# Optimization experiments

Hardware: AMD Instinct MI355X
Metric: run time of the kernel (lower is better)

The kernel has to match this reference:

```python
import jax, jax.numpy as jnp
import numpy as np


def fps(pts, m):
    # pts: [N,3]; iterative farthest point sampling, deterministic start at index 0
    d0 = jnp.sum((pts - pts[0]) ** 2, axis=-1)  # [N]
    def step(mind, _):
        nxt = jnp.argmax(mind)
        d = jnp.sum((pts - pts[nxt]) ** 2, axis=-1)
        return jnp.minimum(mind, d), nxt
    _, idxs = jax.lax.scan(step, d0, None, length=m - 1)
    return jnp.concatenate([jnp.zeros((1,), idxs.dtype), idxs])  # [m]


def knn(queries, pts, k):
    # queries [M,3], pts [N,3] -> [M,k] indices of k nearest points (includes self)
    d = (jnp.sum(queries ** 2, -1, keepdims=True)
         - 2.0 * queries @ pts.T
         + jnp.sum(pts ** 2, -1)[None, :])  # [M,N]
    _, idx = jax.lax.top_k(-d, k)
    return idx


def mlp(x, params):
    # shared PointNet MLP: Linear+ReLU stack
    for w, b in params:
        x = jax.nn.relu(x @ w + b)
    return x


def sa_level(points, feats, ratio, k, params):
    # set-abstraction: fps downsample -> knn group -> shared MLP -> max pool per cluster
    B, N, _ = points.shape
    m = int(N * ratio)
    sel = jax.vmap(lambda p: fps(p, m))(points)                      # [B,m]
    npts = jnp.take_along_axis(points, sel[..., None], axis=1)       # [B,m,3]
    nbr = jax.vmap(knn, in_axes=(0, 0, None))(npts, points, k)       # [B,m,k]
    C = feats.shape[-1]
    kf = jnp.take_along_axis(feats, nbr.reshape(B, m * k, 1), axis=1).reshape(B, m, k, C)
    h = mlp(kf, params)                                              # [B,m,k,out]
    return npts, jnp.max(h, axis=2)                                  # [B,m,3], [B,m,out]


def setup_inputs() -> dict:
    key = jax.random.key(0)
    ks = jax.random.split(key, 20)
    points = jax.random.normal(ks[0], (8, 8192, 3), dtype=jnp.float32)
    batch = jnp.repeat(jnp.arange(8, dtype=jnp.int64), 8192)
    dims = {
        'pn1': [(3, 8), (8, 16), (16, 16)],
        'pn2': [(16, 32), (32, 64), (64, 64)],
        'pn3': [(64, 128), (128, 256), (256, 256)],
    }
    inp = {'points': points, 'batch': batch}
    i = 1
    for name, shapes in dims.items():
        for j, (cin, cout) in enumerate(shapes, start=1):
            inp[f'{name}_w{j}'] = jax.random.normal(ks[i], (cin, cout), dtype=jnp.float32) * (1.0 / np.sqrt(cin))
            inp[f'{name}_b{j}'] = jnp.zeros((cout,), dtype=jnp.float32)
            i += 1
    return inp


def reference(points, batch,
              pn1_w1, pn1_b1, pn1_w2, pn1_b2, pn1_w3, pn1_b3,
              pn2_w1, pn2_b1, pn2_w2, pn2_b2, pn2_w3, pn2_b3,
              pn3_w1, pn3_b1, pn3_w2, pn3_b2, pn3_w3, pn3_b3):
    # batch is implied by the uniform [B,N,3] layout (all clouds equal size)
    p1 = [(pn1_w1, pn1_b1), (pn1_w2, pn1_b2), (pn1_w3, pn1_b3)]
    p2 = [(pn2_w1, pn2_b1), (pn2_w2, pn2_b2), (pn2_w3, pn2_b3)]
    p3 = [(pn3_w1, pn3_b1), (pn3_w2, pn3_b2), (pn3_w3, pn3_b3)]
    pts1, f1 = sa_level(points, points, 0.25, 4, p1)   # [8,2048,3], [8,2048,16]
    pts2, f2 = sa_level(pts1, f1, 0.25, 4, p2)         # [8,512,3], [8,512,64]
    # level 3: cluster == batch -> global max pool per cloud
    out = jnp.max(mlp(f2, p3), axis=1)                  # [8,256]
    return out
```

## Files before the change

kernel.cpp:

```cpp
#include <hip/hip_runtime.h>
#include <stdint.h>

typedef unsigned long long u64;
typedef unsigned int u32;
typedef float f2 __attribute__((ext_vector_type(2)));

__device__ __forceinline__ float rn_mul(float a, float b){ return __fmul_rn(a,b); }
__device__ __forceinline__ float rn_add(float a, float b){ return __fadd_rn(a,b); }
__device__ __forceinline__ float rn_sub(float a, float b){ return __fsub_rn(a,b); }

__device__ __forceinline__ float sq3(float dx, float dy, float dz){
  return rn_add(rn_add(rn_mul(dx,dx), rn_mul(dy,dy)), rn_mul(dz,dz));
}

__device__ __forceinline__ u32 fkey(float d){
  u32 b = __float_as_uint(d);
  return b ^ ((u32)((int)b >> 31) | 0x80000000u);
}
__device__ __forceinline__ float unfkey(u32 k){
  const u32 b = (k & 0x80000000u) ? (k ^ 0x80000000u) : ~k;
  return __uint_as_float(b);
}

__device__ __forceinline__ u64 shfl_xor64(u64 v, int mask){
  int lo = __shfl_xor((int)(u32)v, mask, 64);
  int hi = __shfl_xor((int)(u32)(v >> 32), mask, 64);
  return ((u64)(u32)hi << 32) | (u32)lo;
}
__device__ __forceinline__ u64 umin64(u64 a, u64 b){ return a < b ? a : b; }
__device__ __forceinline__ u64 umax64(u64 a, u64 b){ return a > b ? a : b; }

template<int C>
__device__ __forceinline__ u32 dstep(u32 v){
  u32 x = (u32)__builtin_amdgcn_update_dpp((int)v, (int)v, C, 0xF, 0xF, false);
  return x > v ? x : v;
}
__device__ __forceinline__ u32 wave64_maxu(u32 v){
  v = dstep<0x111>(v);
  v = dstep<0x112>(v);
  v = dstep<0x114>(v);
  v = dstep<0x118>(v);
  v = dstep<0x142>(v);
  v = dstep<0x143>(v);
  return (u32)__builtin_amdgcn_readlane((int)v, 63);
}
template<int C>
__device__ __forceinline__ u64 dstep64(u64 v){
  const u32 l = (u32)__builtin_amdgcn_update_dpp((int)(u32)v, (int)(u32)v, C, 0xF, 0xF, false);
  const u32 h = (u32)__builtin_amdgcn_update_dpp((int)(u32)(v>>32), (int)(u32)(v>>32), C, 0xF, 0xF, false);
  const u64 o = ((u64)h << 32) | l;
  return o > v ? o : v;
}
__device__ __forceinline__ u64 red8_max64(u64 v){
  v = dstep64<0x111>(v);
  v = dstep64<0x112>(v);
  v = dstep64<0x114>(v);
  const u32 l = (u32)__builtin_amdgcn_readlane((int)(u32)v, 7);
  const u32 h = (u32)__builtin_amdgcn_readlane((int)(u32)(v>>32), 7);
  return ((u64)h << 32) | l;
}

template<int N, int NT, int M>
__global__ __launch_bounds__(NT)
void fps_kernel(const float* __restrict__ pts, float* __restrict__ npts)
{
#pragma clang fp contract(off)
  constexpr int NW  = NT / 64;
  constexpr int CAP = 1216;
  constexpr int PPT = 20;
  constexpr int PP2 = PPT / 2;
  __shared__ u32 Sx[NW*CAP], Sy[NW*CAP], Sz[NW*CAP], Sidx[NW*CAP];
  __shared__ u32 cnt[NW];
  __shared__ u32 blo[NW][3], bhi[NW][3];
  __shared__ u64 part[2][NW];
  const int b = blockIdx.x;
  const float* P = pts + (size_t)b * N * 3;
  float* O = npts + (size_t)b * M * 3;
  const int tid = threadIdx.x, lane = tid & 63, wv = tid >> 6;

  if (tid < NW) cnt[tid] = 0;
  if (tid < NW*3){ ((u32*)blo)[tid] = 0xFFFFFFFFu; ((u32*)bhi)[tid] = 0u; }
  __syncthreads();

  for (int i = tid; i < N; i += NT){
    const float x = P[3*i+0], y = P[3*i+1], z = P[3*i+2];
    const int oc = (x < 0.f ? 1 : 0) | (y < 0.f ? 2 : 0) | (z < 0.f ? 4 : 0);
    const u32 s = atomicAdd(&cnt[oc], 1u);
    if (s < CAP){
      Sx[oc*CAP+s] = __float_as_uint(x);
      Sy[oc*CAP+s] = __float_as_uint(y);
      Sz[oc*CAP+s] = __float_as_uint(z);
      Sidx[oc*CAP+s] = (u32)i;
    }
    atomicMin(&blo[oc][0], fkey(x)); atomicMax(&bhi[oc][0], fkey(x));
    atomicMin(&blo[oc][1], fkey(y)); atomicMax(&bhi[oc][1], fkey(y));
    atomicMin(&blo[oc][2], fkey(z)); atomicMax(&bhi[oc][2], fkey(z));
  }
  __syncthreads();

  const u32 cw = cnt[wv];
  const int base = wv * CAP;
  f2 X[PP2], Y[PP2], Z[PP2], MD[PP2];
  u32 OI[PPT];
#pragma unroll
  for (int k = 0; k < PPT; ++k){
    u32 s = (u32)lane + 64u*(u32)k;
    s = (s < cw) ? s : (s - cw);
    const float xx = __uint_as_float(Sx[base+s]);
    const float yy = __uint_as_float(Sy[base+s]);
    const float zz = __uint_as_float(Sz[base+s]);
    OI[k] = Sidx[base+s];
    if (k & 1){ X[k>>1].y = xx; Y[k>>1].y = yy; Z[k>>1].y = zz; }
    else      { X[k>>1].x = xx; Y[k>>1].x = yy; Z[k>>1].x = zz; }
  }
  const float lox = unfkey(blo[wv][0]), loy = unfkey(blo[wv][1]), loz = unfkey(blo[wv][2]);
  const float hix = unfkey(bhi[wv][0]), hiy = unfkey(bhi[wv][1]), hiz = unfkey(bhi[wv][2]);
  __syncthreads();

#pragma unroll
  for (int k = 0; k < PPT; ++k){
    const u32 oi = OI[k];
    const float xx = (k&1) ? X[k>>1].y : X[k>>1].x;
    const float yy = (k&1) ? Y[k>>1].y : Y[k>>1].x;
    const float zz = (k&1) ? Z[k>>1].y : Z[k>>1].x;
    Sx[oi] = __float_as_uint(xx);
    Sy[oi] = __float_as_uint(yy);
    Sz[oi] = __float_as_uint(zz);
  }
  __syncthreads();

#define MAKECAND(dst, wkbits)                                                 \
  {                                                                           \
    u32 mo = 0xFFFFFFFFu;                                                     \
    if (__float_as_uint(bm) == (wkbits)){                                     \
      _Pragma("unroll")                                                       \
      for (int k = 0; k < PPT; ++k){                                          \
        const float mk = (k&1) ? MD[k>>1].y : MD[k>>1].x;                     \
        if (__float_as_uint(mk) == (wkbits)) mo = mo < OI[k] ? mo : OI[k];    \
      }                                                                       \
    }                                                                         \
    (dst) = ~mo;                                                              \
  }

  const float c0x = P[0], c0y = P[1], c0z = P[2];
  float bm = 0.0f;
  {
    const f2 cx2 = {c0x,c0x}, cy2 = {c0y,c0y}, cz2 = {c0z,c0z};
#pragma unroll
    for (int j = 0; j < PP2; ++j){
      const f2 dx = X[j]-cx2, dy = Y[j]-cy2, dz = Z[j]-cz2;
      MD[j] = ((dx*dx) + (dy*dy)) + (dz*dz);
      bm = fmaxf(bm, fmaxf(MD[j].x, MD[j].y));
    }
  }
  if (tid == 0){ O[0]=c0x; O[1]=c0y; O[2]=c0z; }
  u64 mypk;
  {
    const u32 wk = wave64_maxu(__float_as_uint(bm));
    u32 wc; MAKECAND(wc, wk);
    wc = wave64_maxu(wc);
    mypk = ((u64)wk << 32) | wc;
  }

  for (int it = 1; it < M; ++it){
    const int p = it & 1;
    if (lane == 63) part[p][wv] = mypk;
    __syncthreads();
    const u64 best = red8_max64(part[p][lane & (NW-1)]);
    const u32 widx = ~(u32)best;
    const float cx = __uint_as_float(Sx[widx]);
    const float cy = __uint_as_float(Sy[widx]);
    const float cz = __uint_as_float(Sz[widx]);
    if (tid == 0){ O[3*it+0]=cx; O[3*it+1]=cy; O[3*it+2]=cz; }
    const float tdx = fmaxf(0.0f, fmaxf(lox - cx, cx - hix));
    const float tdy = fmaxf(0.0f, fmaxf(loy - cy, cy - hiy));
    const float tdz = fmaxf(0.0f, fmaxf(loz - cz, cz - hiz));
    const float lb2 = ((tdx*tdx + tdy*tdy) + tdz*tdz) * 0.98f;
    const float wkf = __uint_as_float((u32)(mypk >> 32));
    const int doup = __builtin_amdgcn_readfirstlane(lb2 < wkf ? 1 : 0);
    if (doup){
      const f2 cx2 = {cx,cx}, cy2 = {cy,cy}, cz2 = {cz,cz};
      float nbm = 0.0f;
#pragma unroll
      for (int j = 0; j < PP2; ++j){
        const f2 dx = X[j]-cx2, dy = Y[j]-cy2, dz = Z[j]-cz2;
        const f2 d = ((dx*dx) + (dy*dy)) + (dz*dz);
        MD[j].x = fminf(MD[j].x, d.x);
        MD[j].y = fminf(MD[j].y, d.y);
        nbm = fmaxf(nbm, fmaxf(MD[j].x, MD[j].y));
      }
      bm = nbm;
      const u32 wk = wave64_maxu(__float_as_uint(bm));
      u32 wc; MAKECAND(wc, wk);
      wc = wave64_maxu(wc);
      mypk = ((u64)wk << 32) | wc;
    }
  }
#undef MAKECAND
}

__device__ __forceinline__ void top4_insert(u64& a0,u64& a1,u64& a2,u64& a3, u64 p){
  if (p < a3){
    const bool c2 = p < a2, c1 = p < a1, c0 = p < a0;
    const u64 n3 = c2 ? a2 : p;
    const u64 n2 = c2 ? (c1 ? a1 : p) : a2;
    const u64 n1 = c1 ? (c0 ? a0 : p) : a1;
    const u64 n0 = c0 ? p : a0;
    a0=n0; a1=n1; a2=n2; a3=n3;
  }
}

__device__ __forceinline__ void merge4(u64& a0, u64& a1, u64& a2, u64& a3, int st)
{
  const u64 b0 = shfl_xor64(a0, st);
  const u64 b1 = shfl_xor64(a1, st);
  const u64 b2 = shfl_xor64(a2, st);
  const u64 b3 = shfl_xor64(a3, st);
  const u64 m0 = umin64(a0, b3);
  const u64 m1 = umin64(a1, b2);
  const u64 m2 = umin64(a2, b1);
  const u64 m3 = umin64(a3, b0);
  const u64 lo02 = umin64(m0,m2), hi02 = umax64(m0,m2);
  const u64 lo13 = umin64(m1,m3), hi13 = umax64(m1,m3);
  a0 = umin64(lo02, lo13); a1 = umax64(lo02, lo13);
  a2 = umin64(hi02, hi13); a3 = umax64(hi02, hi13);
}

template<int N, int M, int CH>
__global__ __launch_bounds__(256)
void knn_mlp1_kernel(const float* __restrict__ q, const float* __restrict__ pts,
                     const float* __restrict__ w1, const float* __restrict__ b1,
                     const float* __restrict__ w2, const float* __restrict__ b2,
                     const float* __restrict__ w3, const float* __restrict__ b3,
                     float* __restrict__ f1)
{
  __shared__ float4 s4[CH];
  constexpr int QPB = 64;
  const int blk = blockIdx.x;
  const int b = blk / (M / QPB);
  const int chunk = blk % (M / QPB);
  const int tid = threadIdx.x;
  const int g = tid >> 2;
  const int r = tid & 3;
  const int qi = chunk * QPB + g;
  const float* qp = q + ((size_t)b * M + qi) * 3;
  const float qx = qp[0], qy = qp[1], qz = qp[2];
  const float sumq = rn_add(rn_add(rn_mul(qx,qx), rn_mul(qy,qy)), rn_mul(qz,qz));
  const float* P = pts + (size_t)b * N * 3;

  u64 a0=~0ull, a1=~0ull, a2=~0ull, a3=~0ull;
  for (int c0 = 0; c0 < N; c0 += CH){
    for (int i = tid; i < CH; i += 256){
      const float x = P[3*(c0+i)+0], y = P[3*(c0+i)+1], z = P[3*(c0+i)+2];
      s4[i] = make_float4(x, y, z,
          rn_add(rn_add(rn_mul(x,x), rn_mul(y,y)), rn_mul(z,z)));
    }
    __syncthreads();
#pragma unroll 4
    for (int jj = r; jj < CH; jj += 4){
      const float4 v = s4[jj];
      const float dot = rn_add(rn_add(rn_mul(qx,v.x), rn_mul(qy,v.y)),
                               rn_mul(qz,v.z));
      const float d = rn_add(rn_sub(sumq, rn_mul(2.0f, dot)), v.w);
      top4_insert(a0,a1,a2,a3, ((u64)fkey(d) << 32) | (u32)(c0+jj));
    }
    __syncthreads();
  }
  merge4(a0,a1,a2,a3,1);
  merge4(a0,a1,a2,a3,2);
  const u64 selp = (r==0) ? a0 : (r==1) ? a1 : (r==2) ? a2 : a3;
  const u32 nidx = (u32)selp;

  const float nx = P[3*nidx+0], ny = P[3*nidx+1], nz = P[3*nidx+2];
  float h1[8];
#pragma unroll
  for (int c = 0; c < 8; ++c){
    float acc = b1[c];
    acc = fmaf(nx, w1[0*8+c], acc);
    acc = fmaf(ny, w1[1*8+c], acc);
    acc = fmaf(nz, w1[2*8+c], acc);
    h1[c] = fmaxf(acc, 0.0f);
  }
  float h2[16];
#pragma unroll
  for (int c = 0; c < 16; ++c){
    float acc = b2[c];
#pragma unroll
    for (int k = 0; k < 8; ++k) acc = fmaf(h1[k], w2[k*16+c], acc);
    h2[c] = fmaxf(acc, 0.0f);
  }
  float* fo = f1 + ((size_t)b * M + qi) * 16;
#pragma unroll
  for (int c = 0; c < 16; ++c){
    float acc = b3[c];
#pragma unroll
    for (int k = 0; k < 16; ++k) acc = fmaf(h2[k], w3[k*16+c], acc);
    float v = fmaxf(acc, 0.0f);
    v = fmaxf(v, __shfl_xor(v, 1, 64));
    v = fmaxf(v, __shfl_xor(v, 2, 64));
    if (r == 0) fo[c] = v;
  }
}

__global__ __launch_bounds__(256)
void knn_mlp2_kernel(const float* __restrict__ q, const float* __restrict__ pts,
                     const float* __restrict__ f1,
                     const float* __restrict__ w1, const float* __restrict__ b1,
                     const float* __restrict__ w2, const float* __restrict__ b2,
                     const float* __restrict__ w3, const float* __restrict__ b3,
                     float* __restrict__ f2)
{
  constexpr int N = 2048, M = 512, QPB = 64, QSTR = 2048;
  __shared__ float4 s4[N];
  const int blk = blockIdx.x;
  const int b = blk / (M / QPB);
  const int chunk = blk % (M / QPB);
  const int tid = threadIdx.x;
  const int g = tid >> 2;
  const int r = tid & 3;
  const int qi = chunk * QPB + g;
  const float* qp = q + ((size_t)b * QSTR + qi) * 3;
  const float qx = qp[0], qy = qp[1], qz = qp[2];
  const float sumq = rn_add(rn_add(rn_mul(qx,qx), rn_mul(qy,qy)), rn_mul(qz,qz));
  const float* P = pts + (size_t)b * N * 3;

  for (int i = tid; i < N; i += 256){
    const float x = P[3*i+0], y = P[3*i+1], z = P[3*i+2];
    s4[i] = make_float4(x, y, z,
        rn_add(rn_add(rn_mul(x,x), rn_mul(y,y)), rn_mul(z,z)));
  }
  __syncthreads();

  u64 a0=~0ull, a1=~0ull, a2=~0ull, a3=~0ull;
#pragma unroll 4
  for (int j = r; j < N; j += 4){
    const float4 v = s4[j];
    const float dot = rn_add(rn_add(rn_mul(qx,v.x), rn_mul(qy,v.y)),
                             rn_mul(qz,v.z));
    const float d = rn_add(rn_sub(sumq, rn_mul(2.0f, dot)), v.w);
    top4_insert(a0,a1,a2,a3, ((u64)fkey(d) << 32) | (u32)j);
  }
  merge4(a0,a1,a2,a3,1);
  merge4(a0,a1,a2,a3,2);
  const u64 selp = (r==0) ? a0 : (r==1) ? a1 : (r==2) ? a2 : a3;
  const u32 nidx = (u32)selp;

  const float* fv = f1 + ((size_t)b * 2048 + nidx) * 16;
  float x[16];
#pragma unroll
  for (int i = 0; i < 4; ++i){
    const float4 v = ((const float4*)fv)[i];
    x[4*i+0]=v.x; x[4*i+1]=v.y; x[4*i+2]=v.z; x[4*i+3]=v.w;
  }
  float h1[32];
#pragma unroll
  for (int c = 0; c < 32; ++c){
    float acc = b1[c];
#pragma unroll
    for (int k = 0; k < 16; ++k) acc = fmaf(x[k], w1[k*32+c], acc);
    h1[c] = fmaxf(acc, 0.0f);
  }
  float h2[64];
#pragma unroll
  for (int c = 0; c < 64; ++c){
    float acc = b2[c];
#pragma unroll
    for (int k = 0; k < 32; ++k) acc = fmaf(h1[k], w2[k*64+c], acc);
    h2[c] = fmaxf(acc, 0.0f);
  }
  float* fo = f2 + ((size_t)b * M + qi) * 64;
#pragma unroll
  for (int c = 0; c < 64; ++c){
    float acc = b3[c];
#pragma unroll
    for (int k = 0; k < 64; ++k) acc = fmaf(h2[k], w3[k*64+c], acc);
    float v = fmaxf(acc, 0.0f);
    v = fmaxf(v, __shfl_xor(v, 1, 64));
    v = fmaxf(v, __shfl_xor(v, 2, 64));
    if (r == 0) fo[c] = v;
  }
}

__global__ __launch_bounds__(256)
void mlp3_kernel(const float* __restrict__ f2,
                 const float* __restrict__ w1, const float* __restrict__ b1,
                 const float* __restrict__ w2, const float* __restrict__ b2,
                 const float* __restrict__ w3, const float* __restrict__ b3,
                 float* __restrict__ out)
{
  constexpr int P = 16;
  __shared__ float X [P][64];
  __shared__ float H1[P][128];
  __shared__ float H2[P][256];
  __shared__ float PM[4][256];
  const int blk = blockIdx.x;
  const int b  = blk >> 5;
  const int pc = blk & 31;
  const int tid = threadIdx.x;
  const float* F = f2 + ((size_t)b * 512 + (size_t)pc * P) * 64;
  { const float4 v = ((const float4*)F)[tid]; ((float4*)&X[0][0])[tid] = v; }
  __syncthreads();
  {
    const int p = tid >> 4, c0 = (tid & 15) * 8;
    float acc[8];
#pragma unroll
    for (int i = 0; i < 8; ++i) acc[i] = b1[c0+i];
    for (int k = 0; k < 64; ++k){
      const float xv = X[p][k];
      const float4 wa = *(const float4*)&w1[k*128 + c0];
      const float4 wb = *(const float4*)&w1[k*128 + c0 + 4];
      acc[0]=fmaf(xv,wa.x,acc[0]); acc[1]=fmaf(xv,wa.y,acc[1]);
      acc[2]=fmaf(xv,wa.z,acc[2]); acc[3]=fmaf(xv,wa.w,acc[3]);
      acc[4]=fmaf(xv,wb.x,acc[4]); acc[5]=fmaf(xv,wb.y,acc[5]);
      acc[6]=fmaf(xv,wb.z,acc[6]); acc[7]=fmaf(xv,wb.w,acc[7]);
    }
#pragma unroll
    for (int i = 0; i < 8; ++i) H1[p][c0+i] = fmaxf(acc[i], 0.0f);
  }
  __syncthreads();
  {
    const int p = tid >> 4, c0 = (tid & 15) * 16;
    float acc[16];
#pragma unroll
    for (int i = 0; i < 16; ++i) acc[i] = b2[c0+i];
    for (int k = 0; k < 128; ++k){
      const float xv = H1[p][k];
#pragma unroll
      for (int i4 = 0; i4 < 4; ++i4){
        const float4 wv = *(const float4*)&w2[k*256 + c0 + 4*i4];
        acc[4*i4+0]=fmaf(xv,wv.x,acc[4*i4+0]);
        acc[4*i4+1]=fmaf(xv,wv.y,acc[4*i4+1]);
        acc[4*i4+2]=fmaf(xv,wv.z,acc[4*i4+2]);
        acc[4*i4+3]=fmaf(xv,wv.w,acc[4*i4+3]);
      }
    }
#pragma unroll
    for (int i = 0; i < 16; ++i) H2[p][c0+i] = fmaxf(acc[i], 0.0f);
  }
  __syncthreads();
  {
    const int pg = tid >> 6, c0 = (tid & 63) * 4;
    float acc[4][4];
#pragma unroll
    for (int p4 = 0; p4 < 4; ++p4)
#pragma unroll
      for (int i = 0; i < 4; ++i) acc[p4][i] = b3[c0+i];
    for (int k = 0; k < 256; ++k){
      const float4 wv = *(const float4*)&w3[k*256 + c0];
#pragma unroll
      for (int p4 = 0; p4 < 4; ++p4){
        const float xv = H2[pg*4+p4][k];
        acc[p4][0]=fmaf(xv,wv.x,acc[p4][0]);
        acc[p4][1]=fmaf(xv,wv.y,acc[p4][1]);
        acc[p4][2]=fmaf(xv,wv.z,acc[p4][2]);
        acc[p4][3]=fmaf(xv,wv.w,acc[p4][3]);
      }
    }
    float4 mx;
    mx.x = fmaxf(fmaxf(fmaxf(acc[0][0],0.f),fmaxf(acc[1][0],0.f)),
                 fmaxf(fmaxf(acc[2][0],0.f),fmaxf(acc[3][0],0.f)));
    mx.y = fmaxf(fmaxf(fmaxf(acc[0][1],0.f),fmaxf(acc[1][1],0.f)),
                 fmaxf(fmaxf(acc[2][1],0.f),fmaxf(acc[3][1],0.f)));
    mx.z = fmaxf(fmaxf(fmaxf(acc[0][2],0.f),fmaxf(acc[1][2],0.f)),
                 fmaxf(fmaxf(acc[2][2],0.f),fmaxf(acc[3][2],0.f)));
    mx.w = fmaxf(fmaxf(fmaxf(acc[0][3],0.f),fmaxf(acc[1][3],0.f)),
                 fmaxf(fmaxf(acc[2][3],0.f),fmaxf(acc[3][3],0.f)));
    *(float4*)&PM[pg][c0] = mx;
  }
  __syncthreads();
  {
    const float m = fmaxf(fmaxf(PM[0][tid], PM[1][tid]),
                          fmaxf(PM[2][tid], PM[3][tid]));
    atomicMax((int*)(out + b*256 + tid), __float_as_int(m));
  }
}

extern "C" void kernel_launch(void* const* d_in, const int* in_sizes, int n_in,
                              void* d_out, int out_size, void* d_ws, size_t ws_size,
                              hipStream_t stream)
{
  const float* pts  = (const float*)d_in[0];
  const float* p1w1 = (const float*)d_in[2];
  const float* p1b1 = (const float*)d_in[3];
  const float* p1w2 = (const float*)d_in[4];
  const float* p1b2 = (const float*)d_in[5];
  const float* p1w3 = (const float*)d_in[6];
  const float* p1b3 = (const float*)d_in[7];
  const float* p2w1 = (const float*)d_in[8];
  const float* p2b1 = (const float*)d_in[9];
  const float* p2w2 = (const float*)d_in[10];
  const float* p2b2 = (const float*)d_in[11];
  const float* p2w3 = (const float*)d_in[12];
  const float* p2b3 = (const float*)d_in[13];
  const float* p3w1 = (const float*)d_in[14];
  const float* p3b1 = (const float*)d_in[15];
  const float* p3w2 = (const float*)d_in[16];
  const float* p3b2 = (const float*)d_in[17];
  const float* p3w3 = (const float*)d_in[18];
  const float* p3b3 = (const float*)d_in[19];

  float* ws = (float*)d_ws;
  size_t o = 0;
  float* npts1 = ws + o; o += (size_t)8*2048*3;
  float* f1    = ws + o; o += (size_t)8*2048*16;
  float* f2    = ws + o; o += (size_t)8*512*64;

  fps_kernel<8192,512,2048><<<8, 512, 0, stream>>>(pts, npts1);
  knn_mlp1_kernel<8192,2048,2048><<<8*32, 256, 0, stream>>>(npts1, pts,
      p1w1, p1b1, p1w2, p1b2, p1w3, p1b3, f1);
  knn_mlp2_kernel<<<8*8, 256, 0, stream>>>(npts1, npts1, f1,
      p2w1, p2b1, p2w2, p2b2, p2w3, p2b3, f2);
  hipMemsetAsync(d_out, 0, (size_t)out_size * sizeof(float), stream);
  mlp3_kernel<<<8*32, 256, 0, stream>>>(f2,
      p3w1, p3b1, p3w2, p3b2, p3w3, p3b3, (float*)d_out);
}
```

Before: 2.459 ms.

## Pack FPS shared points as float4, tree-reduce max, defer output writes

Replaces the separate x/y/z/idx shared arrays with one float4 array, so the per-iteration centroid fetch becomes a single LDS load. The running max over each thread's distances becomes a pairwise tree instead of a serial chain, shortening the dependency path. Centroid output stores move out of the serial loop: winner indices are recorded in a small shared array and written out in parallel afterwards. CAP/PPT are now derived from N (same values for N=8192). The float4 layout uses more shared memory, and the ushort index array requires N ≤ 65536.

```diff
diff --git a/kernel.cpp b/kernel.cpp
--- a/kernel.cpp
+++ b/kernel.cpp
@@ -60,19 +60,24 @@
   return ((u64)h << 32) | l;
 }
 
+__device__ __forceinline__ f2 f2max(f2 a, f2 b){
+  f2 r; r.x = fmaxf(a.x,b.x); r.y = fmaxf(a.y,b.y); return r;
+}
+
 template<int N, int NT, int M>
 __global__ __launch_bounds__(NT)
 void fps_kernel(const float* __restrict__ pts, float* __restrict__ npts)
 {
 #pragma clang fp contract(off)
   constexpr int NW  = NT / 64;
-  constexpr int CAP = 1216;
-  constexpr int PPT = 20;
-  constexpr int PP2 = PPT / 2;
-  __shared__ u32 Sx[NW*CAP], Sy[NW*CAP], Sz[NW*CAP], Sidx[NW*CAP];
+  constexpr int CAP = N/8 + 192;
+  constexpr int PPT = CAP/64 + 1;
+  constexpr int PP2 = PPT/2;
+  __shared__ float4 SP[NW*CAP];
+  __shared__ unsigned short WX[M];
+  __shared__ u64 part[2][NW];
   __shared__ u32 cnt[NW];
   __shared__ u32 blo[NW][3], bhi[NW][3];
-  __shared__ u64 part[2][NW];
   const int b = blockIdx.x;
   const float* P = pts + (size_t)b * N * 3;
   float* O = npts + (size_t)b * M * 3;
@@ -86,12 +91,7 @@
     const float x = P[3*i+0], y = P[3*i+1], z = P[3*i+2];
     const int oc = (x < 0.f ? 1 : 0) | (y < 0.f ? 2 : 0) | (z < 0.f ? 4 : 0);
     const u32 s = atomicAdd(&cnt[oc], 1u);
-    if (s < CAP){
-      Sx[oc*CAP+s] = __float_as_uint(x);
-      Sy[oc*CAP+s] = __float_as_uint(y);
-      Sz[oc*CAP+s] = __float_as_uint(z);
-      Sidx[oc*CAP+s] = (u32)i;
-    }
+    if (s < CAP) SP[oc*CAP+s] = make_float4(x, y, z, __uint_as_float((u32)i));
     atomicMin(&blo[oc][0], fkey(x)); atomicMax(&bhi[oc][0], fkey(x));
     atomicMin(&blo[oc][1], fkey(y)); atomicMax(&bhi[oc][1], fkey(y));
     atomicMin(&blo[oc][2], fkey(z)); atomicMax(&bhi[oc][2], fkey(z));
@@ -106,12 +106,10 @@
   for (int k = 0; k < PPT; ++k){
     u32 s = (u32)lane + 64u*(u32)k;
     s = (s < cw) ? s : (s - cw);
-    const float xx = __uint_as_float(Sx[base+s]);
-    const float yy = __uint_as_float(Sy[base+s]);
-    const float zz = __uint_as_float(Sz[base+s]);
-    OI[k] = Sidx[base+s];
-    if (k & 1){ X[k>>1].y = xx; Y[k>>1].y = yy; Z[k>>1].y = zz; }
-    else      { X[k>>1].x = xx; Y[k>>1].x = yy; Z[k>>1].x = zz; }
+    const float4 v = SP[base + s];
+    OI[k] = __float_as_uint(v.w);
+    if (k & 1){ X[k>>1].y = v.x; Y[k>>1].y = v.y; Z[k>>1].y = v.z; }
+    else      { X[k>>1].x = v.x; Y[k>>1].x = v.y; Z[k>>1].x = v.z; }
   }
   const float lox = unfkey(blo[wv][0]), loy = unfkey(blo[wv][1]), loz = unfkey(blo[wv][2]);
   const float hix = unfkey(bhi[wv][0]), hiy = unfkey(bhi[wv][1]), hiz = unfkey(bhi[wv][2]);
@@ -119,14 +117,12 @@
 
 #pragma unroll
   for (int k = 0; k < PPT; ++k){
-    const u32 oi = OI[k];
     const float xx = (k&1) ? X[k>>1].y : X[k>>1].x;
     const float yy = (k&1) ? Y[k>>1].y : Y[k>>1].x;
     const float zz = (k&1) ? Z[k>>1].y : Z[k>>1].x;
-    Sx[oi] = __float_as_uint(xx);
-    Sy[oi] = __float_as_uint(yy);
-    Sz[oi] = __float_as_uint(zz);
-  }
+    SP[OI[k]] = make_float4(xx, yy, zz, 0.0f);
+  }
+  if (tid == 0) WX[0] = 0;
   __syncthreads();
 
 #define MAKECAND(dst, wkbits)                                                 \
@@ -142,18 +138,28 @@
     (dst) = ~mo;                                                              \
   }
 
+#define TREEBM(tarr)                                                          \
+  _Pragma("unroll")                                                           \
+  for (int i = 0; i < 5; ++i) tarr[i] = f2max(tarr[i], tarr[i+5]);            \
+  _Pragma("unroll")                                                           \
+  for (int i = 0; i < 2; ++i) tarr[i] = f2max(tarr[i], tarr[i+3]);            \
+  tarr[0] = f2max(tarr[0], tarr[2]);                                          \
+  tarr[0] = f2max(tarr[0], tarr[1]);                                          \
+  bm = fmaxf(tarr[0].x, tarr[0].y);
+
   const float c0x = P[0], c0y = P[1], c0z = P[2];
-  float bm = 0.0f;
+  float bm;
   {
     const f2 cx2 = {c0x,c0x}, cy2 = {c0y,c0y}, cz2 = {c0z,c0z};
+    f2 t[PP2];
 #pragma unroll
     for (int j = 0; j < PP2; ++j){
       const f2 dx = X[j]-cx2, dy = Y[j]-cy2, dz = Z[j]-cz2;
       MD[j] = ((dx*dx) + (dy*dy)) + (dz*dz);
-      bm = fmaxf(bm, fmaxf(MD[j].x, MD[j].y));
-    }
-  }
-  if (tid == 0){ O[0]=c0x; O[1]=c0y; O[2]=c0z; }
+      t[j] = MD[j];
+    }
+    TREEBM(t)
+  }
   u64 mypk;
   {
     const u32 wk = wave64_maxu(__float_as_uint(bm));
@@ -163,40 +169,43 @@
   }
 
   for (int it = 1; it < M; ++it){
-    const int p = it & 1;
-    if (lane == 63) part[p][wv] = mypk;
+    if (lane == 63) part[it & 1][wv] = mypk;
     __syncthreads();
-    const u64 best = red8_max64(part[p][lane & (NW-1)]);
+    const u64 best = red8_max64(part[it & 1][lane & (NW-1)]);
     const u32 widx = ~(u32)best;
-    const float cx = __uint_as_float(Sx[widx]);
-    const float cy = __uint_as_float(Sy[widx]);
-    const float cz = __uint_as_float(Sz[widx]);
-    if (tid == 0){ O[3*it+0]=cx; O[3*it+1]=cy; O[3*it+2]=cz; }
-    const float tdx = fmaxf(0.0f, fmaxf(lox - cx, cx - hix));
-    const float tdy = fmaxf(0.0f, fmaxf(loy - cy, cy - hiy));
-    const float tdz = fmaxf(0.0f, fmaxf(loz - cz, cz - hiz));
+    if (tid == 0) WX[it] = (unsigned short)widx;
+    const float4 c = SP[widx];
+    const float tdx = fmaxf(0.0f, fmaxf(lox - c.x, c.x - hix));
+    const float tdy = fmaxf(0.0f, fmaxf(loy - c.y, c.y - hiy));
+    const float tdz = fmaxf(0.0f, fmaxf(loz - c.z, c.z - hiz));
     const float lb2 = ((tdx*tdx + tdy*tdy) + tdz*tdz) * 0.98f;
     const float wkf = __uint_as_float((u32)(mypk >> 32));
     const int doup = __builtin_amdgcn_readfirstlane(lb2 < wkf ? 1 : 0);
     if (doup){
-      const f2 cx2 = {cx,cx}, cy2 = {cy,cy}, cz2 = {cz,cz};
-      float nbm = 0.0f;
+      const f2 cx2 = {c.x,c.x}, cy2 = {c.y,c.y}, cz2 = {c.z,c.z};
+      f2 t[PP2];
 #pragma unroll
       for (int j = 0; j < PP2; ++j){
         const f2 dx = X[j]-cx2, dy = Y[j]-cy2, dz = Z[j]-cz2;
         const f2 d = ((dx*dx) + (dy*dy)) + (dz*dz);
         MD[j].x = fminf(MD[j].x, d.x);
         MD[j].y = fminf(MD[j].y, d.y);
-        nbm = fmaxf(nbm, fmaxf(MD[j].x, MD[j].y));
+        t[j] = MD[j];
       }
-      bm = nbm;
+      TREEBM(t)
       const u32 wk = wave64_maxu(__float_as_uint(bm));
       u32 wc; MAKECAND(wc, wk);
       wc = wave64_maxu(wc);
       mypk = ((u64)wk << 32) | wc;
     }
   }
+  __syncthreads();
+  for (int j = tid; j < M; j += NT){
+    const float4 v = SP[WX[j]];
+    O[3*j+0] = v.x; O[3*j+1] = v.y; O[3*j+2] = v.z;
+  }
 #undef MAKECAND
+#undef TREEBM
 }
 
 __device__ __forceinline__ void top4_insert(u64& a0,u64& a1,u64& a2,u64& a3, u64 p){
```

Result: no change. 2.476 ms (+0.7%).
